# Kernel tuning notes

Measured on AMD Instinct MI355X. Metric: run time of the kernel, lower is better.

Reference implementation:

```python
import jax, jax.numpy as jnp
import numpy as np

# --- static config (matches init_kwargs) ---
B, IMG = 256, 64
N, W = 128, 20          # num_memory_locations, memory_size
UNITS = 256             # controller LSTM units
R, WH = 1, 1            # read / write heads
SHIFT = 1               # conv shift range -> 3 shift weights
OUT = 8                 # num_bits_per_vector (NTM output dim)
CLIP = 20.0
NH = R + WH
PPH = W + 1 + 1 + (2 * SHIFT + 1) + 1   # k, beta, g, s, gamma per head
EPS = 1e-8
D_IN = 32 + R * W       # CNN feature dim + read vectors into controller


def conv2d(x, w, b):
    y = jax.lax.conv_general_dilated(x, w, window_strides=(1, 1), padding='SAME',
                                     dimension_numbers=('NHWC', 'HWIO', 'NHWC'))
    return jax.nn.relu(y + b)


def maxpool2(x):
    return jax.lax.reduce_window(x, -jnp.inf, jax.lax.max,
                                 window_dimensions=(1, 2, 2, 1),
                                 window_strides=(1, 2, 2, 1), padding='VALID')


def ntm_last_output(seq, lstm_wx, lstm_wh, lstm_b, head_w, head_b, out_w, out_b):
    b = seq.shape[0]
    xs = jnp.transpose(seq, (1, 0, 2))  # [T, B, 32]
    h0 = jnp.zeros((b, UNITS), seq.dtype)
    carry0 = (h0, h0,
              jnp.full((b, R, W), 1e-6, seq.dtype),      # read vectors
              jnp.full((b, NH, N), 1.0 / N, seq.dtype),  # head weightings
              jnp.full((b, N, W), 1e-6, seq.dtype))      # memory matrix

    def step(carry, xt):
        h, c, reads, w_prev, M = carry
        # controller LSTM
        ci = jnp.concatenate([xt, reads.reshape(b, R * W)], axis=-1)
        z = ci @ lstm_wx + h @ lstm_wh + lstm_b
        zi, zf, zg, zo = jnp.split(z, 4, axis=-1)
        c = jax.nn.sigmoid(zf) * c + jax.nn.sigmoid(zi) * jnp.tanh(zg)
        h = jax.nn.sigmoid(zo) * jnp.tanh(c)
        # head parameters
        p = jnp.clip(h @ head_w + head_b, -CLIP, CLIP)
        hp = p[:, :NH * PPH].reshape(b, NH, PPH)
        k = jnp.tanh(hp[..., :W])
        beta = jax.nn.softplus(hp[..., W])
        gate = jax.nn.sigmoid(hp[..., W + 1])
        s = jax.nn.softmax(hp[..., W + 2:W + 2 + 2 * SHIFT + 1], axis=-1)
        gamma = jax.nn.softplus(hp[..., -1]) + 1.0
        # content addressing: cosine-similarity softmax
        Mn = M / (jnp.linalg.norm(M, axis=-1, keepdims=True) + EPS)
        kn = k / (jnp.linalg.norm(k, axis=-1, keepdims=True) + EPS)
        sim = jnp.einsum('bhw,bnw->bhn', kn, Mn)
        wc = jax.nn.softmax(beta[..., None] * sim, axis=-1)
        # location addressing: interpolate, circular shift, sharpen
        wg = gate[..., None] * wc + (1.0 - gate[..., None]) * w_prev
        wt = sum(s[..., d + SHIFT][..., None] * jnp.roll(wg, d, axis=-1)
                 for d in range(-SHIFT, SHIFT + 1))
        wp = (wt + EPS) ** gamma[..., None]
        w = wp / wp.sum(axis=-1, keepdims=True)
        # read from prev memory
        reads = jnp.einsum('brn,bnw->brw', w[:, :R], M)
        # write (erase then add)
        ea = p[:, NH * PPH:].reshape(b, WH, 2 * W)
        e = jax.nn.sigmoid(ea[..., :W])
        a = jnp.tanh(ea[..., W:])
        for j in range(WH):
            ww = w[:, R + j][..., None]  # [B, N, 1]
            M = M * (1.0 - ww * e[:, j][:, None, :]) + ww * a[:, j][:, None, :]
        out = jnp.clip(jnp.concatenate([h, reads.reshape(b, R * W)], axis=-1) @ out_w + out_b,
                       -CLIP, CLIP)
        return (h, c, reads, w, M), out

    _, ys = jax.lax.scan(step, carry0, xs)
    return ys[-1]  # return_sequences=False -> last step output [B, OUT]


def setup_inputs():
    key = jax.random.key(0)
    ks = jax.random.split(key, 10)
    g = lambda k, shp, sc: jax.random.normal(k, shp, jnp.float32) * sc
    return {
        'inputs': jax.random.normal(ks[0], (B, IMG, IMG), jnp.float32),
        'conv1_w': g(ks[1], (3, 3, 1, 16), 0.3),
        'conv1_b': jnp.zeros((16,), jnp.float32),
        'conv2_w': g(ks[2], (3, 3, 16, 32), 0.1),
        'conv2_b': jnp.zeros((32,), jnp.float32),
        'lstm_wx': g(ks[3], (D_IN, 4 * UNITS), 0.08),
        'lstm_wh': g(ks[4], (UNITS, 4 * UNITS), 0.08),
        'lstm_b': jnp.zeros((4 * UNITS,), jnp.float32),
        'head_w': g(ks[5], (UNITS, NH * PPH + 2 * W * WH), 0.05),
        'head_b': jnp.zeros((NH * PPH + 2 * W * WH,), jnp.float32),
        'out_w': g(ks[6], (UNITS + R * W, OUT), 0.1),
        'out_b': jnp.zeros((OUT,), jnp.float32),
        'dense_w': g(ks[7], (OUT, 2), 0.3),
        'dense_b': jnp.zeros((2,), jnp.float32),
    }


def reference(inputs, conv1_w, conv1_b, conv2_w, conv2_b,
              lstm_wx, lstm_wh, lstm_b, head_w, head_b,
              out_w, out_b, dense_w, dense_b):
    x = inputs.reshape(-1, IMG, IMG, 1)
    x = maxpool2(conv2d(x, conv1_w, conv1_b))
    x = maxpool2(conv2d(x, conv2_w, conv2_b))
    seq = x.reshape(x.shape[0], x.shape[1] * x.shape[2], 32)  # [B, 256, 32]
    last = ntm_last_output(seq, lstm_wx, lstm_wh, lstm_b, head_w, head_b, out_w, out_b)
    return jax.nn.softmax(last @ dense_w + dense_b, axis=-1)
```

## Files before the change

### kernel.cpp

```cpp
#include <hip/hip_runtime.h>
#include <hip/hip_fp16.h>
#include <cstdint>
#include <cstddef>


#define MW    20
#define NLOC  128
#define ZC    1024
#define PC    92
#define CLIPV 20.0f

__device__ __forceinline__ float sigmoidf_(float x) { return 1.0f / (1.0f + expf(-x)); }
__device__ __forceinline__ float softplusf_(float x) { return log1pf(expf(x)); }

__device__ __forceinline__ float dot2f(uint32_t w, uint32_t a, float c) {
    asm("v_dot2_f32_f16 %0, %1, %2, %0" : "+v"(c) : "v"(w), "v"(a));
    return c;
}

__device__ __forceinline__ float wvalA(const float* wx, const float* wh, int k, int col) {
    return (k < 32) ? wx[k * ZC + col] : wh[(k - 32) * ZC + col];
}
__device__ __forceinline__ uint32_t packA(const float* wx, const float* wh, int pr, int col) {
    __half2 h = __floats2half2_rn(wvalA(wx, wh, 2 * pr, col), wvalA(wx, wh, 2 * pr + 1, col));
    return *reinterpret_cast<uint32_t*>(&h);
}

__global__ __launch_bounds__(256) void prep_pack(const float* __restrict__ wx,
                                                 const float* __restrict__ wh,
                                                 const float* __restrict__ hw,
                                                 uint32_t* __restrict__ WG8,
                                                 uint32_t* __restrict__ WrT,
                                                 uint32_t* __restrict__ hw2) {
    int idx = blockIdx.x * 256 + threadIdx.x;
    if (idx < 147456) {
        int m = idx & 3, c = (idx >> 2) & 127, j = (idx >> 9) & 1, pr = idx >> 10;
        WG8[idx] = packA(wx, wh, pr, 8 * c + 4 * j + m);
    } else if (idx < 159744) {
        int q2 = idx - 147456;
        int col = q2 / 12, q = q2 - col * 12;
        if (q < 10) {
            __half2 h = __floats2half2_rn(wx[(32 + 2 * q) * ZC + col], wx[(33 + 2 * q) * ZC + col]);
            WrT[q2] = *reinterpret_cast<uint32_t*>(&h);
        } else WrT[q2] = 0u;
    } else if (idx < 171520) {
        int q3 = idx - 159744;
        int up = q3 / 92, col = q3 - up * 92;
        __half2 h = __floats2half2_rn(hw[(2 * up) * PC + col], hw[(2 * up + 1) * PC + col]);
        hw2[q3] = *reinterpret_cast<uint32_t*>(&h);
    }
}

__global__ __launch_bounds__(256) void conv1_pool(const float* __restrict__ in,
                                                  const float* __restrict__ w,
                                                  const float* __restrict__ bias,
                                                  float* __restrict__ out) {
    int idx = blockIdx.x * 256 + threadIdx.x;
    if (idx >= 256 * 32 * 32 * 16) return;
    int c = idx & 15, x = (idx >> 4) & 31, y = (idx >> 9) & 31, b = idx >> 14;
    const float* inb = in + (size_t)b * 4096;
    float bv = bias[c];
    float mx = 0.0f;
    #pragma unroll
    for (int dy = 0; dy < 2; ++dy)
    #pragma unroll
    for (int dx = 0; dx < 2; ++dx) {
        int oy = 2 * y + dy, ox = 2 * x + dx;
        float s = bv;
        #pragma unroll
        for (int ky = 0; ky < 3; ++ky) {
            int iy = oy + ky - 1;
            if (iy < 0 || iy > 63) continue;
            #pragma unroll
            for (int kx = 0; kx < 3; ++kx) {
                int ix = ox + kx - 1;
                if (ix < 0 || ix > 63) continue;
                s = fmaf(inb[iy * 64 + ix], w[(ky * 3 + kx) * 16 + c], s);
            }
        }
        mx = fmaxf(mx, fmaxf(s, 0.0f));
    }
    out[idx] = mx;
}

__global__ __launch_bounds__(256) void conv2_pool(const float* __restrict__ p1,
                                                  const float* __restrict__ w,
                                                  const float* __restrict__ bias,
                                                  float* __restrict__ seq) {
    int idx = blockIdx.x * 256 + threadIdx.x;
    if (idx >= 256 * 16 * 16 * 32) return;
    int c = idx & 31, x = (idx >> 5) & 15, y = (idx >> 9) & 15, b = idx >> 13;
    const float* pb = p1 + (size_t)b * (32 * 32 * 16);
    float bv = bias[c];
    float acc[4] = {bv, bv, bv, bv};
    #pragma unroll
    for (int ky = 0; ky < 3; ++ky)
    #pragma unroll
    for (int kx = 0; kx < 3; ++kx) {
        float w16[16];
        #pragma unroll
        for (int i = 0; i < 16; ++i) w16[i] = w[((ky * 3 + kx) * 16 + i) * 32 + c];
        #pragma unroll
        for (int dy = 0; dy < 2; ++dy)
        #pragma unroll
        for (int dx = 0; dx < 2; ++dx) {
            int iy = 2 * y + dy + ky - 1, ix = 2 * x + dx + kx - 1;
            if (iy < 0 || iy > 31 || ix < 0 || ix > 31) continue;
            const float4* pin4 = (const float4*)(pb + (iy * 32 + ix) * 16);
            float4 v0 = pin4[0], v1 = pin4[1], v2 = pin4[2], v3 = pin4[3];
            int a = dy * 2 + dx;
            acc[a] = fmaf(v0.x, w16[0], acc[a]);  acc[a] = fmaf(v0.y, w16[1], acc[a]);
            acc[a] = fmaf(v0.z, w16[2], acc[a]);  acc[a] = fmaf(v0.w, w16[3], acc[a]);
            acc[a] = fmaf(v1.x, w16[4], acc[a]);  acc[a] = fmaf(v1.y, w16[5], acc[a]);
            acc[a] = fmaf(v1.z, w16[6], acc[a]);  acc[a] = fmaf(v1.w, w16[7], acc[a]);
            acc[a] = fmaf(v2.x, w16[8], acc[a]);  acc[a] = fmaf(v2.y, w16[9], acc[a]);
            acc[a] = fmaf(v2.z, w16[10], acc[a]); acc[a] = fmaf(v2.w, w16[11], acc[a]);
            acc[a] = fmaf(v3.x, w16[12], acc[a]); acc[a] = fmaf(v3.y, w16[13], acc[a]);
            acc[a] = fmaf(v3.z, w16[14], acc[a]); acc[a] = fmaf(v3.w, w16[15], acc[a]);
        }
    }
    float mx = 0.0f;
    #pragma unroll
    for (int a = 0; a < 4; ++a) mx = fmaxf(mx, acc[a]);
    seq[idx] = mx;
}

#define PSCLIP1(col_) fminf(fmaxf(pp[0][col_] + pp[1][col_] + pp[2][col_] + pp[3][col_] + hb[col_], -CLIPV), CLIPV)

__global__ __launch_bounds__(1024, 4) void ntm_scan13(
    const float* __restrict__ seq,
    const uint32_t* __restrict__ WG8,
    const uint32_t* __restrict__ WrT,
    const uint32_t* __restrict__ hw2G,
    const float* __restrict__ lb,
    const float* __restrict__ hb,
    const float* __restrict__ ow,
    const float* __restrict__ ob,
    const float* __restrict__ dw,
    const float* __restrict__ db,
    float* __restrict__ out)
{
    __shared__ uint4 Wl4[32 * 2 * 128];
    __shared__ float zpart[4][ZC];
    __shared__ __align__(16) uint32_t aci[160];
    __shared__ uint32_t xbuf[16];
    __shared__ float Msh[MW][132];
    __shared__ float wprev[2][NLOC];
    __shared__ float pp[4][PC];
    __shared__ float evs[MW], avs[MW], rds[MW];
    __shared__ uint32_t rp[10];
    __shared__ float o8[8];
    __shared__ int sflag;

    const int t = threadIdx.x;
    const int bb = blockIdx.x;
    const uint4* WGV = (const uint4*)WG8;

    for (int i = t; i < 8192; i += 1024) {
        int lp = i >> 8, j = (i >> 7) & 1, c = i & 127;
        int gp = (lp >> 3) * 36 + (lp & 7);
        Wl4[i] = WGV[(gp * 2 + j) * 128 + c];
    }

    if (t < 160) {
        uint32_t v = 0u;
        if (t < 16) {
            __half2 hh2 = __floats2half2_rn(seq[(size_t)bb * 8192 + 2 * t],
                                            seq[(size_t)bb * 8192 + 2 * t + 1]);
            v = *reinterpret_cast<uint32_t*>(&hh2);
        }
        aci[t] = v;
    }
    for (int i = t; i < MW * 132; i += 1024)
        Msh[i / 132][i - (i / 132) * 132] = 1e-6f;
    if (t < 256) wprev[t >> 7][t & 127] = 1.0f / 128.0f;
    if (t < 10) {
        __half2 hh2 = __floats2half2_rn(1e-6f, 1e-6f);
        rp[t] = *reinterpret_cast<uint32_t*>(&hh2);
    }
    if (t == 0) sflag = 0;
    float c_reg = 0.0f;
    __syncthreads();

    int svc = 0;
    auto subsync = [&]() {
        svc += 6;
        __threadfence_block();
        if ((t & 63) == 0)
            __hip_atomic_fetch_add(&sflag, 1, __ATOMIC_RELAXED, __HIP_MEMORY_SCOPE_WORKGROUP);
        while (__hip_atomic_load(&sflag, __ATOMIC_RELAXED, __HIP_MEMORY_SCOPE_WORKGROUP) < svc)
            __builtin_amdgcn_s_sleep(1);
        __threadfence_block();
    };

    auto doP3 = [&](int pt) {
        if (pt < 368) {
            int kq2 = pt / 92, col = pt - kq2 * 92;
            const uint32_t* hwp = hw2G + kq2 * 32 * 92 + col;
            const uint32_t* hbp = aci + 16 + kq2 * 32;
            float s = 0.0f;
            #pragma unroll 8
            for (int uu = 0; uu < 32; ++uu)
                s = dot2f(hwp[uu * 92], hbp[uu], s);
            pp[kq2][col] = s;
        }
    };
    auto doP4 = [&](int pt) {
        if (pt < 128) {
            const int l = pt & 63, hh = pt >> 6;
            const int hc = hh * 26;
            float beta  = softplusf_(PSCLIP1(hc + 20));
            float gte   = sigmoidf_(PSCLIP1(hc + 21));
            float s0r = PSCLIP1(hc + 22), s1r = PSCLIP1(hc + 23), s2r = PSCLIP1(hc + 24);
            float mS = fmaxf(s0r, fmaxf(s1r, s2r));
            float q0 = expf(s0r - mS), q1 = expf(s1r - mS), q2 = expf(s2r - mS);
            float qin = 1.0f / (q0 + q1 + q2);
            float sh0 = q0 * qin, sh1 = q1 * qin, sh2 = q2 * qin;
            float gamma = softplusf_(PSCLIP1(hc + 25)) + 1.0f;

            float kvv = (l < 20) ? tanhf(PSCLIP1(hc + l)) : 0.0f;
            float kn2 = kvv * kvv;
            #pragma unroll
            for (int o = 1; o < 64; o <<= 1) kn2 += __shfl_xor(kn2, o, 64);
            float kden = sqrtf(kn2) + 1e-8f;

            float d0 = 0, d1 = 0, m20 = 0, m21 = 0;
            #pragma unroll
            for (int wi = 0; wi < 20; ++wi) {
                float kk = __shfl(kvv, wi, 64);
                float2 mv = *reinterpret_cast<const float2*>(&Msh[wi][2 * l]);
                d0  = fmaf(kk, mv.x, d0);      d1  = fmaf(kk, mv.y, d1);
                m20 = fmaf(mv.x, mv.x, m20);   m21 = fmaf(mv.y, mv.y, m21);
            }
            float x0 = beta * (d0 / ((sqrtf(m20) + 1e-8f) * kden));
            float x1 = beta * (d1 / ((sqrtf(m21) + 1e-8f) * kden));
            float mx = fmaxf(x0, x1);
            #pragma unroll
            for (int o = 1; o < 64; o <<= 1) mx = fmaxf(mx, __shfl_xor(mx, o, 64));
            float e0 = expf(x0 - mx), e1 = expf(x1 - mx);
            float se = e0 + e1;
            #pragma unroll
            for (int o = 1; o < 64; o <<= 1) se += __shfl_xor(se, o, 64);
            float inv = 1.0f / se;
            float2 wpv = *reinterpret_cast<const float2*>(&wprev[hh][2 * l]);
            float wg0 = gte * (e0 * inv) + (1.0f - gte) * wpv.x;
            float wg1 = gte * (e1 * inv) + (1.0f - gte) * wpv.y;
            float wgm = __shfl(wg1, (l + 63) & 63, 64);
            float wgp = __shfl(wg0, (l + 1) & 63, 64);
            float wt0 = sh0 * wg1 + sh1 * wg0 + sh2 * wgm;
            float wt1 = sh0 * wgp + sh1 * wg1 + sh2 * wg0;
            float wpw0 = expf(gamma * logf(wt0 + 1e-8f));
            float wpw1 = expf(gamma * logf(wt1 + 1e-8f));
            float ssum = wpw0 + wpw1;
            #pragma unroll
            for (int o = 1; o < 64; o <<= 1) ssum += __shfl_xor(ssum, o, 64);
            float rin = 1.0f / ssum;
            *reinterpret_cast<float2*>(&wprev[hh][2 * l]) = make_float2(wpw0 * rin, wpw1 * rin);
        } else if (pt < 168) {
            int r2 = pt - 128;
            if (r2 < 20) evs[r2]      = sigmoidf_(PSCLIP1(52 + r2));
            else         avs[r2 - 20] = tanhf(PSCLIP1(72 + (r2 - 20)));
        }
    };
    auto doP5 = [&](int pt) {
        if (pt < 320) {
            int wi = pt >> 4, l16 = pt & 15;
            int n0 = l16 * 8;
            float ev = evs[wi], av = avs[wi];
            float s = 0.0f;
            #pragma unroll
            for (int n = n0; n < n0 + 8; ++n) {
                float mv = Msh[wi][n];
                s = fmaf(wprev[0][n], mv, s);
                float wwn = wprev[1][n];
                Msh[wi][n] = mv * (1.0f - wwn * ev) + wwn * av;
            }
            s += __shfl_xor(s, 1, 64); s += __shfl_xor(s, 2, 64);
            s += __shfl_xor(s, 4, 64); s += __shfl_xor(s, 8, 64);
            float sodd = __shfl_xor(s, 16, 64);
            if (l16 == 0) {
                rds[wi] = s;
                if ((wi & 1) == 0) {
                    __half2 hp = __floats2half2_rn(s, sodd);
                    rp[wi >> 1] = *reinterpret_cast<uint32_t*>(&hp);
                }
            }
        }
    };

    for (int i = 0; i < 256; ++i) {
        if (t < 512) {
            const int kq = t >> 7, c = t & 127;
            const int prb = kq * 36;
            float a0 = 0, a1 = 0, a2 = 0, a3 = 0, a4 = 0, a5 = 0, a6 = 0, a7 = 0;
            const uint4* cap = (const uint4*)(aci + prb);
            #pragma unroll
            for (int g = 0; g < 9; ++g) {
                uint4 A = cap[g];
                uint32_t aa[4] = {A.x, A.y, A.z, A.w};
                #pragma unroll
                for (int q = 0; q < 4; ++q) {
                    const int p = g * 4 + q;
                    uint4 w0, w1;
                    if (p < 8) {
                        w0 = Wl4[((kq * 8 + p) * 2 + 0) * 128 + c];
                        w1 = Wl4[((kq * 8 + p) * 2 + 1) * 128 + c];
                    } else {
                        w0 = WGV[((prb + p) * 2 + 0) * 128 + c];
                        w1 = WGV[((prb + p) * 2 + 1) * 128 + c];
                    }
                    a0 = dot2f(w0.x, aa[q], a0); a1 = dot2f(w0.y, aa[q], a1);
                    a2 = dot2f(w0.z, aa[q], a2); a3 = dot2f(w0.w, aa[q], a3);
                    a4 = dot2f(w1.x, aa[q], a4); a5 = dot2f(w1.y, aa[q], a5);
                    a6 = dot2f(w1.z, aa[q], a6); a7 = dot2f(w1.w, aa[q], a7);
                }
            }
            *reinterpret_cast<float4*>(&zpart[kq][8 * c])     = make_float4(a0, a1, a2, a3);
            *reinterpret_cast<float4*>(&zpart[kq][8 * c + 4]) = make_float4(a4, a5, a6, a7);
        } else if (t < 896) {
            if (i > 0) {
                const int pt = t - 512;
                doP3(pt);
                subsync();
                doP4(pt);
                subsync();
                doP5(pt);
            }
        } else if (t < 912 && i < 255) {
            int j = t - 896;
            const float* xp = seq + (size_t)bb * 8192 + (size_t)(i + 1) * 32 + 2 * j;
            __half2 hh2 = __floats2half2_rn(xp[0], xp[1]);
            xbuf[j] = *reinterpret_cast<uint32_t*>(&hh2);
        }
        __syncthreads();

        if (t < 256) {
            uint32_t rp0 = rp[0], rp1 = rp[1], rp2 = rp[2], rp3 = rp[3];
            uint32_t rp4 = rp[4], rp5 = rp[5], rp6 = rp[6], rp7 = rp[7];
            uint32_t rp8 = rp[8], rp9 = rp[9];
            float zg4[4];
            #pragma unroll
            for (int g4 = 0; g4 < 4; ++g4) {
                const uint4* wp = (const uint4*)(WrT + ((g4 << 8) + t) * 12);
                uint4 A = wp[0], B = wp[1], C = wp[2];
                float s = 0.0f;
                s = dot2f(A.x, rp0, s); s = dot2f(A.y, rp1, s);
                s = dot2f(A.z, rp2, s); s = dot2f(A.w, rp3, s);
                s = dot2f(B.x, rp4, s); s = dot2f(B.y, rp5, s);
                s = dot2f(B.z, rp6, s); s = dot2f(B.w, rp7, s);
                s = dot2f(C.x, rp8, s); s = dot2f(C.y, rp9, s);
                zg4[g4] = s;
            }
            float zi = lb[t]       + zg4[0] + zpart[0][t]       + zpart[1][t]       + zpart[2][t]       + zpart[3][t];
            float zf = lb[256 + t] + zg4[1] + zpart[0][256 + t] + zpart[1][256 + t] + zpart[2][256 + t] + zpart[3][256 + t];
            float zg = lb[512 + t] + zg4[2] + zpart[0][512 + t] + zpart[1][512 + t] + zpart[2][512 + t] + zpart[3][512 + t];
            float zo = lb[768 + t] + zg4[3] + zpart[0][768 + t] + zpart[1][768 + t] + zpart[2][768 + t] + zpart[3][768 + t];
            float cg = sigmoidf_(zf) * c_reg + sigmoidf_(zi) * tanhf(zg);
            c_reg = cg;
            reinterpret_cast<_Float16*>(aci)[32 + t] = (_Float16)(sigmoidf_(zo) * tanhf(cg));
        } else if (t >= 256 && t < 272 && i < 255) {
            aci[t - 256] = xbuf[t - 256];
        }
        __syncthreads();
    }

    if (t >= 512 && t < 896) {
        const int pt = t - 512;
        doP3(pt);
        subsync();
        doP4(pt);
        subsync();
        doP5(pt);
    }
    __syncthreads();

    if (t < 8) {
        float s = ob[t];
        const _Float16* hrow = reinterpret_cast<const _Float16*>(aci);
        for (int u = 0; u < 256; ++u) s = fmaf((float)hrow[32 + u], ow[u * 8 + t], s);
        #pragma unroll
        for (int wi = 0; wi < 20; ++wi) s = fmaf(rds[wi], ow[(256 + wi) * 8 + t], s);
        o8[t] = fminf(fmaxf(s, -CLIPV), CLIPV);
    }
    __syncthreads();
    if (t == 0) {
        float l0 = db[0], l1 = db[1];
        #pragma unroll
        for (int k = 0; k < 8; ++k) {
            float v = o8[k];
            l0 = fmaf(v, dw[k * 2 + 0], l0);
            l1 = fmaf(v, dw[k * 2 + 1], l1);
        }
        float m = fmaxf(l0, l1);
        float q0 = expf(l0 - m), q1 = expf(l1 - m);
        float inv = 1.0f / (q0 + q1);
        out[bb * 2 + 0] = q0 * inv;
        out[bb * 2 + 1] = q1 * inv;
    }
}

extern "C" void kernel_launch(void* const* d_in, const int* in_sizes, int n_in,
                              void* d_out, int out_size, void* d_ws, size_t ws_size,
                              hipStream_t stream) {
    const float* inputs = (const float*)d_in[0];
    const float* c1w = (const float*)d_in[1];
    const float* c1b = (const float*)d_in[2];
    const float* c2w = (const float*)d_in[3];
    const float* c2b = (const float*)d_in[4];
    const float* lwx = (const float*)d_in[5];
    const float* lwh = (const float*)d_in[6];
    const float* lb  = (const float*)d_in[7];
    const float* hw  = (const float*)d_in[8];
    const float* hb  = (const float*)d_in[9];
    const float* ow  = (const float*)d_in[10];
    const float* ob  = (const float*)d_in[11];
    const float* dw  = (const float*)d_in[12];
    const float* db  = (const float*)d_in[13];
    float* out = (float*)d_out;

    float* ws  = (float*)d_ws;
    float* p1  = ws;
    float* seq = ws + 4194304;
    uint32_t* WG8  = (uint32_t*)(ws + 6291456);
    uint32_t* WrT  = WG8 + 147456;
    uint32_t* hw2G = WrT + 12288;

    hipLaunchKernelGGL(prep_pack,   dim3(670),   dim3(256),  0, stream, lwx, lwh, hw, WG8, WrT, hw2G);
    hipLaunchKernelGGL(conv1_pool,  dim3(16384), dim3(256),  0, stream, inputs, c1w, c1b, p1);
    hipLaunchKernelGGL(conv2_pool,  dim3(8192),  dim3(256),  0, stream, p1, c2w, c2b, seq);
    hipLaunchKernelGGL(ntm_scan13,  dim3(256),   dim3(1024), 0, stream,
                       seq, WG8, WrT, hw2G, lb, hb, ow, ob, dw, db, out);
}
```

Before: 1.935 ms.

## Software-pipeline global weight loads in LSTM gate matvec and coalesce WrT layout

The gate matvec loop now prefetches the next group of global (cache-resident) fp16 weights into registers while computing on the current group, so global-load latency overlaps the dot2 work. The read-vector weight table WrT is relaid out so consecutive threads read consecutive uint4s instead of strided 48-byte records, which coalesces those loads. The spin-wait sleep between sub-phase syncs also grows from 1 to 2. The prefetch adds register pressure under a 1024-thread launch bound, which could force spills.

Result: slower. 5.851 ms (+202.3%).

```diff
diff --git a/kernel.cpp b/kernel.cpp
--- a/kernel.cpp
+++ b/kernel.cpp
@@ -38,7 +38,8 @@
         WG8[idx] = packA(wx, wh, pr, 8 * c + 4 * j + m);
     } else if (idx < 159744) {
         int q2 = idx - 147456;
-        int col = q2 / 12, q = q2 - col * 12;
+        int qq = q2 & 3, col = (q2 >> 2) & 1023, j = q2 >> 12;
+        int q = j * 4 + qq;
         if (q < 10) {
             __half2 h = __floats2half2_rn(wx[(32 + 2 * q) * ZC + col], wx[(33 + 2 * q) * ZC + col]);
             WrT[q2] = *reinterpret_cast<uint32_t*>(&h);
@@ -127,7 +128,13 @@
 
 #define PSCLIP1(col_) fminf(fmaxf(pp[0][col_] + pp[1][col_] + pp[2][col_] + pp[3][col_] + hb[col_], -CLIPV), CLIPV)
 
-__global__ __launch_bounds__(1024, 4) void ntm_scan13(
+#define D8(w0_, w1_, av_) \
+    a0 = dot2f(w0_.x, av_, a0); a1 = dot2f(w0_.y, av_, a1); \
+    a2 = dot2f(w0_.z, av_, a2); a3 = dot2f(w0_.w, av_, a3); \
+    a4 = dot2f(w1_.x, av_, a4); a5 = dot2f(w1_.y, av_, a5); \
+    a6 = dot2f(w1_.z, av_, a6); a7 = dot2f(w1_.w, av_, a7);
+
+__global__ __launch_bounds__(1024, 4) void ntm_scan14(
     const float* __restrict__ seq,
     const uint32_t* __restrict__ WG8,
     const uint32_t* __restrict__ WrT,
@@ -189,7 +196,7 @@
         if ((t & 63) == 0)
             __hip_atomic_fetch_add(&sflag, 1, __ATOMIC_RELAXED, __HIP_MEMORY_SCOPE_WORKGROUP);
         while (__hip_atomic_load(&sflag, __ATOMIC_RELAXED, __HIP_MEMORY_SCOPE_WORKGROUP) < svc)
-            __builtin_amdgcn_s_sleep(1);
+            __builtin_amdgcn_s_sleep(2);
         __threadfence_block();
     };
 
@@ -294,26 +301,43 @@
             const int prb = kq * 36;
             float a0 = 0, a1 = 0, a2 = 0, a3 = 0, a4 = 0, a5 = 0, a6 = 0, a7 = 0;
             const uint4* cap = (const uint4*)(aci + prb);
-            #pragma unroll
-            for (int g = 0; g < 9; ++g) {
+
+            uint4 p0a, p0b, p1a, p1b, p2a, p2b, p3a, p3b;
+            {
+                const uint4* wgp = WGV + (size_t)(prb + 8) * 256 + c;
+                p0a = wgp[0];   p0b = wgp[128];
+                p1a = wgp[256]; p1b = wgp[384];
+                p2a = wgp[512]; p2b = wgp[640];
+                p3a = wgp[768]; p3b = wgp[896];
+            }
+
+            {
+                uint4 A0 = cap[0], A1 = cap[1];
+                uint32_t act[8] = {A0.x, A0.y, A0.z, A0.w, A1.x, A1.y, A1.z, A1.w};
+                #pragma unroll
+                for (int p = 0; p < 8; ++p) {
+                    uint4 w0 = Wl4[((kq * 8 + p) * 2 + 0) * 128 + c];
+                    uint4 w1 = Wl4[((kq * 8 + p) * 2 + 1) * 128 + c];
+                    D8(w0, w1, act[p])
+                }
+            }
+
+            #pragma unroll
+            for (int g = 2; g < 9; ++g) {
+                uint4 w0a = p0a, w0b = p0b, w1a = p1a, w1b = p1b;
+                uint4 w2a = p2a, w2b = p2b, w3a = p3a, w3b = p3b;
+                if (g < 8) {
+                    const uint4* wgp = WGV + (size_t)(prb + (g + 1) * 4) * 256 + c;
+                    p0a = wgp[0];   p0b = wgp[128];
+                    p1a = wgp[256]; p1b = wgp[384];
+                    p2a = wgp[512]; p2b = wgp[640];
+                    p3a = wgp[768]; p3b = wgp[896];
+                }
                 uint4 A = cap[g];
-                uint32_t aa[4] = {A.x, A.y, A.z, A.w};
-                #pragma unroll
-                for (int q = 0; q < 4; ++q) {
-                    const int p = g * 4 + q;
-                    uint4 w0, w1;
-                    if (p < 8) {
-                        w0 = Wl4[((kq * 8 + p) * 2 + 0) * 128 + c];
-                        w1 = Wl4[((kq * 8 + p) * 2 + 1) * 128 + c];
-                    } else {
-                        w0 = WGV[((prb + p) * 2 + 0) * 128 + c];
-                        w1 = WGV[((prb + p) * 2 + 1) * 128 + c];
-                    }
-                    a0 = dot2f(w0.x, aa[q], a0); a1 = dot2f(w0.y, aa[q], a1);
-                    a2 = dot2f(w0.z, aa[q], a2); a3 = dot2f(w0.w, aa[q], a3);
-                    a4 = dot2f(w1.x, aa[q], a4); a5 = dot2f(w1.y, aa[q], a5);
-                    a6 = dot2f(w1.z, aa[q], a6); a7 = dot2f(w1.w, aa[q], a7);
-                }
+                D8(w0a, w0b, A.x)
+                D8(w1a, w1b, A.y)
+                D8(w2a, w2b, A.z)
+                D8(w3a, w3b, A.w)
             }
             *reinterpret_cast<float4*>(&zpart[kq][8 * c])     = make_float4(a0, a1, a2, a3);
             *reinterpret_cast<float4*>(&zpart[kq][8 * c + 4]) = make_float4(a4, a5, a6, a7);
@@ -338,11 +362,14 @@
             uint32_t rp0 = rp[0], rp1 = rp[1], rp2 = rp[2], rp3 = rp[3];
             uint32_t rp4 = rp[4], rp5 = rp[5], rp6 = rp[6], rp7 = rp[7];
             uint32_t rp8 = rp[8], rp9 = rp[9];
+            const uint4* wrt4 = (const uint4*)WrT;
             float zg4[4];
             #pragma unroll
             for (int g4 = 0; g4 < 4; ++g4) {
-                const uint4* wp = (const uint4*)(WrT + ((g4 << 8) + t) * 12);
-                uint4 A = wp[0], B = wp[1], C = wp[2];
+                const int colu = (g4 << 8) + t;
+                uint4 A = wrt4[colu];
+                uint4 B = wrt4[1024 + colu];
+                uint4 C = wrt4[2048 + colu];
                 float s = 0.0f;
                 s = dot2f(A.x, rp0, s); s = dot2f(A.y, rp1, s);
                 s = dot2f(A.z, rp2, s); s = dot2f(A.w, rp3, s);
@@ -428,6 +455,6 @@
     hipLaunchKernelGGL(prep_pack,   dim3(670),   dim3(256),  0, stream, lwx, lwh, hw, WG8, WrT, hw2G);
     hipLaunchKernelGGL(conv1_pool,  dim3(16384), dim3(256),  0, stream, inputs, c1w, c1b, p1);
     hipLaunchKernelGGL(conv2_pool,  dim3(8192),  dim3(256),  0, stream, p1, c2w, c2b, seq);
-    hipLaunchKernelGGL(ntm_scan13,  dim3(256),   dim3(1024), 0, stream,
+    hipLaunchKernelGGL(ntm_scan14,  dim3(256),   dim3(1024), 0, stream,
                        seq, WG8, WrT, hw2G, lb, hb, ow, ob, dw, db, out);
 }
```

## Rebalance NTM scan threads: six gate-matvec slices, four-wave head pipeline

Applied to the files above, without the earlier changes.

The per-step LSTM gate matvec is now split across six K-slices (768 threads) instead of four (512), so each thread does fewer dot2 steps, with fewer weight pairs cached in LDS per slice. The head/memory pipeline shrinks to four waves (256 threads), each doing twice the work in the head projection and memory update, and the input prefetch moves into that group. The read-vector weight table is re-laid out so loads across threads coalesce. The trade-off is shorter matvec chains against a longer serial head/memory critical path and a larger share of weights read from global memory each step.

After: 3.701 ms. +91.2%, slower.

```diff
diff --git a/kernel.cpp b/kernel.cpp
--- a/kernel.cpp
+++ b/kernel.cpp
@@ -38,7 +38,8 @@
         WG8[idx] = packA(wx, wh, pr, 8 * c + 4 * j + m);
     } else if (idx < 159744) {
         int q2 = idx - 147456;
-        int col = q2 / 12, q = q2 - col * 12;
+        int qq = q2 & 3, col = (q2 >> 2) & 1023, j = q2 >> 12;
+        int q = j * 4 + qq;
         if (q < 10) {
             __half2 h = __floats2half2_rn(wx[(32 + 2 * q) * ZC + col], wx[(33 + 2 * q) * ZC + col]);
             WrT[q2] = *reinterpret_cast<uint32_t*>(&h);
@@ -125,9 +126,15 @@
     seq[idx] = mx;
 }
 
-#define PSCLIP1(col_) fminf(fmaxf(pp[0][col_] + pp[1][col_] + pp[2][col_] + pp[3][col_] + hb[col_], -CLIPV), CLIPV)
-
-__global__ __launch_bounds__(1024, 4) void ntm_scan13(
+#define PSCLIP1(col_) fminf(fmaxf(pp[0][col_] + pp[1][col_] + hb[col_], -CLIPV), CLIPV)
+
+#define D8(w0_, w1_, av_) \
+    a0 = dot2f(w0_.x, av_, a0); a1 = dot2f(w0_.y, av_, a1); \
+    a2 = dot2f(w0_.z, av_, a2); a3 = dot2f(w0_.w, av_, a3); \
+    a4 = dot2f(w1_.x, av_, a4); a5 = dot2f(w1_.y, av_, a5); \
+    a6 = dot2f(w1_.z, av_, a6); a7 = dot2f(w1_.w, av_, a7);
+
+__global__ __launch_bounds__(1024, 4) void ntm_scan15(
     const float* __restrict__ seq,
     const uint32_t* __restrict__ WG8,
     const uint32_t* __restrict__ WrT,
@@ -140,13 +147,13 @@
     const float* __restrict__ db,
     float* __restrict__ out)
 {
-    __shared__ uint4 Wl4[32 * 2 * 128];
-    __shared__ float zpart[4][ZC];
+    __shared__ uint4 Wl4[24 * 2 * 128];
+    __shared__ float zpart[6][ZC];
     __shared__ __align__(16) uint32_t aci[160];
     __shared__ uint32_t xbuf[16];
     __shared__ float Msh[MW][132];
     __shared__ float wprev[2][NLOC];
-    __shared__ float pp[4][PC];
+    __shared__ float pp[2][PC];
     __shared__ float evs[MW], avs[MW], rds[MW];
     __shared__ uint32_t rp[10];
     __shared__ float o8[8];
@@ -156,9 +163,9 @@
     const int bb = blockIdx.x;
     const uint4* WGV = (const uint4*)WG8;
 
-    for (int i = t; i < 8192; i += 1024) {
+    for (int i = t; i < 6144; i += 1024) {
         int lp = i >> 8, j = (i >> 7) & 1, c = i & 127;
-        int gp = (lp >> 3) * 36 + (lp & 7);
+        int gp = (lp >> 2) * 24 + (lp & 3);
         Wl4[i] = WGV[(gp * 2 + j) * 128 + c];
     }
 
@@ -184,23 +191,23 @@
 
     int svc = 0;
     auto subsync = [&]() {
-        svc += 6;
+        svc += 4;
         __threadfence_block();
         if ((t & 63) == 0)
             __hip_atomic_fetch_add(&sflag, 1, __ATOMIC_RELAXED, __HIP_MEMORY_SCOPE_WORKGROUP);
         while (__hip_atomic_load(&sflag, __ATOMIC_RELAXED, __HIP_MEMORY_SCOPE_WORKGROUP) < svc)
-            __builtin_amdgcn_s_sleep(1);
+            __builtin_amdgcn_s_sleep(2);
         __threadfence_block();
     };
 
     auto doP3 = [&](int pt) {
-        if (pt < 368) {
+        if (pt < 184) {
             int kq2 = pt / 92, col = pt - kq2 * 92;
-            const uint32_t* hwp = hw2G + kq2 * 32 * 92 + col;
-            const uint32_t* hbp = aci + 16 + kq2 * 32;
+            const uint32_t* hwp = hw2G + kq2 * 64 * 92 + col;
+            const uint32_t* hbp = aci + 16 + kq2 * 64;
             float s = 0.0f;
             #pragma unroll 8
-            for (int uu = 0; uu < 32; ++uu)
+            for (int uu = 0; uu < 64; ++uu)
                 s = dot2f(hwp[uu * 92], hbp[uu], s);
             pp[kq2][col] = s;
         }
@@ -256,29 +263,28 @@
             for (int o = 1; o < 64; o <<= 1) ssum += __shfl_xor(ssum, o, 64);
             float rin = 1.0f / ssum;
             *reinterpret_cast<float2*>(&wprev[hh][2 * l]) = make_float2(wpw0 * rin, wpw1 * rin);
-        } else if (pt < 168) {
+        } else if (pt < 168 + 40) {
             int r2 = pt - 128;
             if (r2 < 20) evs[r2]      = sigmoidf_(PSCLIP1(52 + r2));
-            else         avs[r2 - 20] = tanhf(PSCLIP1(72 + (r2 - 20)));
+            else if (r2 < 40) avs[r2 - 20] = tanhf(PSCLIP1(72 + (r2 - 20)));
         }
     };
     auto doP5 = [&](int pt) {
-        if (pt < 320) {
-            int wi = pt >> 4, l16 = pt & 15;
-            int n0 = l16 * 8;
+        if (pt < 160) {
+            int wi = pt >> 3, l8 = pt & 7;
+            int n0 = l8 * 16;
             float ev = evs[wi], av = avs[wi];
             float s = 0.0f;
             #pragma unroll
-            for (int n = n0; n < n0 + 8; ++n) {
+            for (int n = n0; n < n0 + 16; ++n) {
                 float mv = Msh[wi][n];
                 s = fmaf(wprev[0][n], mv, s);
                 float wwn = wprev[1][n];
                 Msh[wi][n] = mv * (1.0f - wwn * ev) + wwn * av;
             }
-            s += __shfl_xor(s, 1, 64); s += __shfl_xor(s, 2, 64);
-            s += __shfl_xor(s, 4, 64); s += __shfl_xor(s, 8, 64);
-            float sodd = __shfl_xor(s, 16, 64);
-            if (l16 == 0) {
+            s += __shfl_xor(s, 1, 64); s += __shfl_xor(s, 2, 64); s += __shfl_xor(s, 4, 64);
+            float sodd = __shfl_xor(s, 8, 64);
+            if (l8 == 0) {
                 rds[wi] = s;
                 if ((wi & 1) == 0) {
                     __half2 hp = __floats2half2_rn(s, sodd);
@@ -289,48 +295,46 @@
     };
 
     for (int i = 0; i < 256; ++i) {
-        if (t < 512) {
-            const int kq = t >> 7, c = t & 127;
-            const int prb = kq * 36;
+        if (t < 768) {
+            const int s6 = t >> 7, c = t & 127;
+            const int prb = s6 * 24;
             float a0 = 0, a1 = 0, a2 = 0, a3 = 0, a4 = 0, a5 = 0, a6 = 0, a7 = 0;
             const uint4* cap = (const uint4*)(aci + prb);
             #pragma unroll
-            for (int g = 0; g < 9; ++g) {
+            for (int g = 0; g < 6; ++g) {
                 uint4 A = cap[g];
                 uint32_t aa[4] = {A.x, A.y, A.z, A.w};
                 #pragma unroll
                 for (int q = 0; q < 4; ++q) {
                     const int p = g * 4 + q;
                     uint4 w0, w1;
-                    if (p < 8) {
-                        w0 = Wl4[((kq * 8 + p) * 2 + 0) * 128 + c];
-                        w1 = Wl4[((kq * 8 + p) * 2 + 1) * 128 + c];
+                    if (p < 4) {
+                        w0 = Wl4[((s6 * 4 + p) * 2 + 0) * 128 + c];
+                        w1 = Wl4[((s6 * 4 + p) * 2 + 1) * 128 + c];
                     } else {
                         w0 = WGV[((prb + p) * 2 + 0) * 128 + c];
                         w1 = WGV[((prb + p) * 2 + 1) * 128 + c];
                     }
-                    a0 = dot2f(w0.x, aa[q], a0); a1 = dot2f(w0.y, aa[q], a1);
-                    a2 = dot2f(w0.z, aa[q], a2); a3 = dot2f(w0.w, aa[q], a3);
-                    a4 = dot2f(w1.x, aa[q], a4); a5 = dot2f(w1.y, aa[q], a5);
-                    a6 = dot2f(w1.z, aa[q], a6); a7 = dot2f(w1.w, aa[q], a7);
+                    D8(w0, w1, aa[q])
                 }
             }
-            *reinterpret_cast<float4*>(&zpart[kq][8 * c])     = make_float4(a0, a1, a2, a3);
-            *reinterpret_cast<float4*>(&zpart[kq][8 * c + 4]) = make_float4(a4, a5, a6, a7);
-        } else if (t < 896) {
+            *reinterpret_cast<float4*>(&zpart[s6][8 * c])     = make_float4(a0, a1, a2, a3);
+            *reinterpret_cast<float4*>(&zpart[s6][8 * c + 4]) = make_float4(a4, a5, a6, a7);
+        } else {
+            const int pt = t - 768;
+            if (i > 0) doP3(pt);
+            if (pt >= 192 && pt < 208 && i < 255) {
+                int j = pt - 192;
+                const float* xp = seq + (size_t)bb * 8192 + (size_t)(i + 1) * 32 + 2 * j;
+                __half2 hh2 = __floats2half2_rn(xp[0], xp[1]);
+                xbuf[j] = *reinterpret_cast<uint32_t*>(&hh2);
+            }
             if (i > 0) {
-                const int pt = t - 512;
-                doP3(pt);
                 subsync();
                 doP4(pt);
                 subsync();
                 doP5(pt);
             }
-        } else if (t < 912 && i < 255) {
-            int j = t - 896;
-            const float* xp = seq + (size_t)bb * 8192 + (size_t)(i + 1) * 32 + 2 * j;
-            __half2 hh2 = __floats2half2_rn(xp[0], xp[1]);
-            xbuf[j] = *reinterpret_cast<uint32_t*>(&hh2);
         }
         __syncthreads();
 
@@ -338,11 +342,14 @@
             uint32_t rp0 = rp[0], rp1 = rp[1], rp2 = rp[2], rp3 = rp[3];
             uint32_t rp4 = rp[4], rp5 = rp[5], rp6 = rp[6], rp7 = rp[7];
             uint32_t rp8 = rp[8], rp9 = rp[9];
+            const uint4* wrt4 = (const uint4*)WrT;
             float zg4[4];
             #pragma unroll
             for (int g4 = 0; g4 < 4; ++g4) {
-                const uint4* wp = (const uint4*)(WrT + ((g4 << 8) + t) * 12);
-                uint4 A = wp[0], B = wp[1], C = wp[2];
+                const int colu = (g4 << 8) + t;
+                uint4 A = wrt4[colu];
+                uint4 B = wrt4[1024 + colu];
+                uint4 C = wrt4[2048 + colu];
                 float s = 0.0f;
                 s = dot2f(A.x, rp0, s); s = dot2f(A.y, rp1, s);
                 s = dot2f(A.z, rp2, s); s = dot2f(A.w, rp3, s);
@@ -351,10 +358,15 @@
                 s = dot2f(C.x, rp8, s); s = dot2f(C.y, rp9, s);
                 zg4[g4] = s;
             }
-            float zi = lb[t]       + zg4[0] + zpart[0][t]       + zpart[1][t]       + zpart[2][t]       + zpart[3][t];
-            float zf = lb[256 + t] + zg4[1] + zpart[0][256 + t] + zpart[1][256 + t] + zpart[2][256 + t] + zpart[3][256 + t];
-            float zg = lb[512 + t] + zg4[2] + zpart[0][512 + t] + zpart[1][512 + t] + zpart[2][512 + t] + zpart[3][512 + t];
-            float zo = lb[768 + t] + zg4[3] + zpart[0][768 + t] + zpart[1][768 + t] + zpart[2][768 + t] + zpart[3][768 + t];
+            float zi = lb[t]       + zg4[0];
+            float zf = lb[256 + t] + zg4[1];
+            float zg = lb[512 + t] + zg4[2];
+            float zo = lb[768 + t] + zg4[3];
+            #pragma unroll
+            for (int q = 0; q < 6; ++q) {
+                zi += zpart[q][t];       zf += zpart[q][256 + t];
+                zg += zpart[q][512 + t]; zo += zpart[q][768 + t];
+            }
             float cg = sigmoidf_(zf) * c_reg + sigmoidf_(zi) * tanhf(zg);
             c_reg = cg;
             reinterpret_cast<_Float16*>(aci)[32 + t] = (_Float16)(sigmoidf_(zo) * tanhf(cg));
@@ -364,8 +376,8 @@
         __syncthreads();
     }
 
-    if (t >= 512 && t < 896) {
-        const int pt = t - 512;
+    if (t >= 768) {
+        const int pt = t - 768;
         doP3(pt);
         subsync();
         doP4(pt);
@@ -428,6 +440,6 @@
     hipLaunchKernelGGL(prep_pack,   dim3(670),   dim3(256),  0, stream, lwx, lwh, hw, WG8, WrT, hw2G);
     hipLaunchKernelGGL(conv1_pool,  dim3(16384), dim3(256),  0, stream, inputs, c1w, c1b, p1);
     hipLaunchKernelGGL(conv2_pool,  dim3(8192),  dim3(256),  0, stream, p1, c2w, c2b, seq);
-    hipLaunchKernelGGL(ntm_scan13,  dim3(256),   dim3(1024), 0, stream,
+    hipLaunchKernelGGL(ntm_scan15,  dim3(256),   dim3(1024), 0, stream,
                        seq, WG8, WrT, hw2G, lb, hb, ow, ob, dw, db, out);
 }
```
